# Kernel tuning notes

Measured on AMD Instinct MI355X. Metric: run time of the kernel, lower is better.

The kernel has to match this reference:

```python
import jax, jax.numpy as jnp
import numpy as np

K_MASK = -2.3819763e+38
ROPE_BASE = 10000
QUERY_SCALE = 0.08838834764831845  # head_dim ** -0.5, head_dim=128
SOFT_CAP = 50.0
SLIDING_WINDOW = 1024
NUM_HEADS = 32
NUM_KV_HEADS = 8


def apply_rope(inputs, positions, base_frequency=ROPE_BASE):
    # inputs: [B, L, N, H], positions: [B, L]
    head_dim = inputs.shape[-1]
    fraction = 2 * jnp.arange(0, head_dim // 2) / head_dim
    timescale = base_frequency ** fraction
    sinusoid = positions[..., None] / timescale[None, None, :]
    sinusoid = sinusoid[..., None, :]  # [B, L, 1, H/2]
    sin = jnp.sin(sinusoid)
    cos = jnp.cos(sinusoid)
    first, second = jnp.split(inputs, 2, axis=-1)
    out = jnp.concatenate([first * cos - second * sin,
                           second * cos + first * sin], axis=-1)
    return out.astype(inputs.dtype)


def setup_inputs() -> dict:
    key = jax.random.key(0)
    ks = jax.random.split(key, 4)
    B, S, D, N, K, H = 1, 2048, 4096, NUM_HEADS, NUM_KV_HEADS, 128
    x = jax.random.normal(ks[0], (B, S, D), dtype=jnp.float32)
    segment_pos = jnp.broadcast_to(jnp.arange(S, dtype=jnp.int32)[None, :], (B, S))
    # causal mask [B, T, S]
    attn_mask = jnp.broadcast_to(jnp.tril(jnp.ones((S, S), dtype=bool))[None], (B, S, S))
    sd = 1.0 / np.sqrt(D)
    q_w = jax.random.normal(ks[1], (N, D, H), dtype=jnp.float32) * sd
    kv_w = jax.random.normal(ks[2], (2, K, D, H), dtype=jnp.float32) * sd
    out_w = jax.random.normal(ks[3], (N, H, D), dtype=jnp.float32) * (1.0 / np.sqrt(N * H))
    return {"x": x, "segment_pos": segment_pos, "attn_mask": attn_mask,
            "q_w": q_w, "kv_w": kv_w, "out_w": out_w}


def reference(x, segment_pos, attn_mask, q_w, kv_w, out_w):
    B, T, D = x.shape
    N, _, H = q_w.shape
    K = kv_w.shape[1]
    G = N // K

    q = jnp.einsum('BTD,NDH->BTNH', x, q_w)
    k = jnp.einsum('BSD,KDH->BSKH', x, kv_w[0])
    v = jnp.einsum('BSD,KDH->BSKH', x, kv_w[1])

    q = apply_rope(q, segment_pos)
    q = q * QUERY_SCALE
    k = apply_rope(k, segment_pos)

    # GQA logits: [B, T, K, G, S] -> [B, T, N, S]
    qg = q.reshape(B, T, K, G, H)
    logits = jnp.einsum('BTKGH,BSKH->BTKGS', qg, k).reshape(B, T, N, T)

    # soft cap
    logits = jnp.tanh(logits / SOFT_CAP) * SOFT_CAP

    # sliding-window mask (no cache: end_index=0, cache positions = arange)
    cache_positions = jnp.arange(T)[None, None, :]          # [1, 1, S]
    sp = segment_pos[:, :, None]                             # [B, T, 1]
    sliding = (cache_positions > sp - SLIDING_WINDOW) & (cache_positions < sp + SLIDING_WINDOW)
    mask = attn_mask & sliding                               # [B, T, S]

    padded = jnp.where(mask[:, :, None, :], logits, K_MASK)
    probs = jax.nn.softmax(padded, axis=-1).astype(k.dtype)

    pg = probs.reshape(B, T, K, G, T)
    encoded = jnp.einsum('BTKGS,BSKH->BTKGH', pg, v).reshape(B, T, N, H)
    out = jnp.einsum('BTNH,NHD->BTD', encoded, out_w)
    return out
```

## Files before the change

### kernel.cpp

```cpp
#include <hip/hip_runtime.h>
#include <stdint.h>

#define SEQ     2048
#define DMODEL  4096
#define NHEADS  32
#define NKV     8
#define HD      128
#define NQKV    6144
#define K_MASK_F (-2.3819763e+38f)
#define QSCALE   0.08838834764831845f

typedef __attribute__((ext_vector_type(8))) short short8;
typedef __attribute__((ext_vector_type(4))) short short4v;
typedef __attribute__((ext_vector_type(4))) float f32x4;

__device__ __forceinline__ short f2bf(float f) {
  unsigned u = __float_as_uint(f);
  unsigned r = (u + 0x7fffu + ((u >> 16) & 1u)) >> 16;
  return (short)r;
}
__device__ __forceinline__ float bf2f(short s) {
  return __uint_as_float(((unsigned)(unsigned short)s) << 16);
}
__device__ __forceinline__ void split_bf(float v, short& h, short& l) {
  h = f2bf(v);
  l = f2bf(v - bf2f(h));
}
__device__ __forceinline__ f32x4 mfma16(short8 a, short8 b, f32x4 c) {
  return __builtin_amdgcn_mfma_f32_16x16x32_bf16(a, b, c, 0, 0, 0);
}
__device__ __forceinline__ void async16(void* lds, const void* g) {
  __builtin_amdgcn_global_load_lds(
      (const __attribute__((address_space(1))) unsigned int*)g,
      (__attribute__((address_space(3))) unsigned int*)lds, 16, 0, 0);
}
__device__ __forceinline__ float softcap(float s) {
  float e = __expf(s * 0.04f);
  return 50.f - 100.f * __builtin_amdgcn_rcpf(e + 1.f);
}

__global__ void cvt_split_kernel(const float* __restrict__ src, short* __restrict__ hi,
                                 short* __restrict__ lo, int n4) {
  int i = blockIdx.x * blockDim.x + threadIdx.x;
  if (i >= n4) return;
  float4 v = ((const float4*)src)[i];
  float vv[4] = {v.x, v.y, v.z, v.w};
  short hh[4], ll[4];
#pragma unroll
  for (int j = 0; j < 4; ++j) split_bf(vv[j], hh[j], ll[j]);
  short4v h = {hh[0], hh[1], hh[2], hh[3]};
  short4v l = {ll[0], ll[1], ll[2], ll[3]};
  ((short4v*)hi)[i] = h;
  ((short4v*)lo)[i] = l;
}

__global__ void tcvt_kernel(const float* __restrict__ src, long srcSlab, int srcStride,
                            short* __restrict__ dhi, short* __restrict__ dlo,
                            long dstSlab, int dstStride) {
  __shared__ float tile[32][33];
  const float* s = src + (long)blockIdx.z * srcSlab;
  long dbase = (long)blockIdx.z * dstSlab;
  int tx = threadIdx.x & 31, ty = threadIdx.x >> 5;
  int c0 = blockIdx.x * 32, r0 = blockIdx.y * 32;
#pragma unroll
  for (int i = 0; i < 32; i += 8)
    tile[ty + i][tx] = s[(long)(r0 + ty + i) * srcStride + (c0 + tx)];
  __syncthreads();
#pragma unroll
  for (int i = 0; i < 32; i += 8) {
    float v = tile[tx][ty + i];
    long o = dbase + (long)(c0 + ty + i) * dstStride + (r0 + tx);
    short h, l;
    split_bf(v, h, l);
    dhi[o] = h;
    dlo[o] = l;
  }
}

__global__ __launch_bounds__(256)
void gemm3_kernel(const short* __restrict__ Ah, const short* __restrict__ Al,
                  const short* __restrict__ Bh, const short* __restrict__ Bl,
                  float* __restrict__ C, int K, int ldc) {
  __shared__ short lds[4 * 128 * 32];
  const int tid = threadIdx.x;
  const int wave = tid >> 6, lane = tid & 63;
  const int r16 = lane & 15, g4 = lane >> 4;
  const int bm = blockIdx.x, bn = blockIdx.y;
  const int wr = wave >> 1, wc = wave & 1;

  const f32x4 zero = {0.f, 0.f, 0.f, 0.f};
  f32x4 acc[4][4];
#pragma unroll
  for (int m = 0; m < 4; ++m)
#pragma unroll
    for (int n = 0; n < 4; ++n) acc[m][n] = zero;

  const short* gsrc[4] = {Ah, Al, Bh, Bl};
  const int rowbase[4] = {bm * 128, bm * 128, bn * 128, bn * 128};
  const int stgrow = tid >> 2;
  const int stgseg = tid & 3;
  const int nk = K >> 5;

  for (int kt = 0; kt < nk; ++kt) {
    __syncthreads();
#pragma unroll
    for (int b = 0; b < 4; ++b) {
#pragma unroll
      for (int rnd = 0; rnd < 2; ++rnd) {
        int row = rnd * 64 + stgrow;
        const short* g = gsrc[b] + (long)(rowbase[b] + row) * K + kt * 32 + stgseg * 8;
        short* l = lds + b * 4096 + rnd * 2048 + wave * 512;
        async16(l, g);
      }
    }
    __syncthreads();

    short8 afh[4], afl[4], bfh[4], bfl[4];
#pragma unroll
    for (int m = 0; m < 4; ++m) {
      int r = wr * 64 + m * 16 + r16;
      afh[m] = *(const short8*)&lds[0 * 4096 + r * 32 + g4 * 8];
      afl[m] = *(const short8*)&lds[1 * 4096 + r * 32 + g4 * 8];
    }
#pragma unroll
    for (int n = 0; n < 4; ++n) {
      int r = wc * 64 + n * 16 + r16;
      bfh[n] = *(const short8*)&lds[2 * 4096 + r * 32 + g4 * 8];
      bfl[n] = *(const short8*)&lds[3 * 4096 + r * 32 + g4 * 8];
    }
#pragma unroll
    for (int m = 0; m < 4; ++m)
#pragma unroll
      for (int n = 0; n < 4; ++n) {
        acc[m][n] = mfma16(afh[m], bfh[n], acc[m][n]);
        acc[m][n] = mfma16(afh[m], bfl[n], acc[m][n]);
        acc[m][n] = mfma16(afl[m], bfh[n], acc[m][n]);
      }
  }
#pragma unroll
  for (int m = 0; m < 4; ++m)
#pragma unroll
    for (int n = 0; n < 4; ++n) {
      int row = bm * 128 + wr * 64 + m * 16 + g4 * 4;
      int col = bn * 128 + wc * 64 + n * 16 + r16;
#pragma unroll
      for (int r = 0; r < 4; ++r) C[(long)(row + r) * ldc + col] = acc[m][n][r];
    }
}

__global__ void rope_cvt_kernel(const float* __restrict__ qkv, short* __restrict__ qh,
                                short* __restrict__ ql, short* __restrict__ kh,
                                short* __restrict__ kl) {
  int idx = blockIdx.x * 256 + threadIdx.x;
  const int QP = NHEADS * SEQ * 64;
  float first, second, scale;
  long obase;
  int t, hp;
  short *oh, *ol;
  if (idx < QP) {
    int n = idx >> 17;
    int rem = idx & 131071;
    t = rem >> 6;
    hp = rem & 63;
    const float* p = qkv + (long)t * NQKV + n * HD + hp;
    first = p[0];
    second = p[64];
    oh = qh; ol = ql;
    obase = ((long)n * SEQ + t) * HD + hp;
    scale = QSCALE;
  } else {
    int j = idx - QP;
    int kvh = j >> 17;
    int rem = j & 131071;
    t = rem >> 6;
    hp = rem & 63;
    const float* p = qkv + (long)t * NQKV + DMODEL + kvh * HD + hp;
    first = p[0];
    second = p[64];
    oh = kh; ol = kl;
    obase = ((long)kvh * SEQ + t) * HD + hp;
    scale = 1.0f;
  }
  float ts = powf(10000.0f, (float)hp * (1.0f / 64.0f));
  float ang = (float)t / ts;
  float sn, cs;
  sincosf(ang, &sn, &cs);
  float o1 = (first * cs - second * sn) * scale;
  float o2 = (second * cs + first * sn) * scale;
  short h, l;
  split_bf(o1, h, l); oh[obase] = h;      ol[obase] = l;
  split_bf(o2, h, l); oh[obase + 64] = h; ol[obase + 64] = l;
}

__global__ __launch_bounds__(256)
void attn_kernel(const short* __restrict__ qh, const short* __restrict__ ql,
                 const short* __restrict__ kh, const short* __restrict__ kl,
                 const short* __restrict__ vth, const short* __restrict__ vtl,
                 short* __restrict__ ench, short* __restrict__ encl) {
  __shared__ short kt[2][2][32 * 128];
  __shared__ short plds[4][2][512];
  const int n = blockIdx.x;
  const int qt = (int)(__brev(blockIdx.y) >> 27);
  const int tid = threadIdx.x;
  const int wave = tid >> 6, lane = tid & 63;
  const int kv = n >> 2;
  const int T0 = qt * 64;
  const int wq0 = T0 + wave * 16;
  const int r16 = lane & 15, g4 = lane >> 4;

  short8 qfh[4], qfl[4];
  {
    const short* bh = qh + ((long)(n * SEQ + wq0 + r16)) * HD + g4 * 8;
    const short* bl = ql + ((long)(n * SEQ + wq0 + r16)) * HD + g4 * 8;
#pragma unroll
    for (int ks = 0; ks < 4; ++ks) {
      qfh[ks] = *(const short8*)(bh + ks * 32);
      qfl[ks] = *(const short8*)(bl + ks * 32);
    }
  }

  const f32x4 zero = {0.f, 0.f, 0.f, 0.f};
  f32x4 o[8];
#pragma unroll
  for (int i = 0; i < 8; ++i) o[i] = zero;
  float m[4] = {-INFINITY, -INFINITY, -INFINITY, -INFINITY};
  float lsum[4] = {0.f, 0.f, 0.f, 0.f};

  short* pwh = &plds[wave][0][0];
  short* pwl = &plds[wave][1][0];

  const int strow = tid >> 4;
  const int stcol = (((tid & 15) ^ (strow & 7)) << 3);
  const short* kgh = kh + (long)kv * SEQ * HD;
  const short* kgl = kl + (long)kv * SEQ * HD;

  int slo = T0 - 1023;
  if (slo < 0) slo = 0;
  slo &= ~31;
  const int steps = (T0 + 64 - slo) >> 5;

  auto stage = [&](int sc, int kbuf) {
#pragma unroll
    for (int c = 0; c < 2; ++c) {
      int row = c * 16 + strow;
      async16(&kt[kbuf][0][c * 2048 + tid * 8], kgh + (long)(sc + row) * HD + stcol);
      async16(&kt[kbuf][1][c * 2048 + tid * 8], kgl + (long)(sc + row) * HD + stcol);
    }
  };

  int buf = 0;
  stage(slo, 0);
  __syncthreads();

  for (int i = 0; i < steps; ++i) {
    const int sc = slo + (i << 5);
    if (i + 1 < steps) stage(sc + 32, buf ^ 1);
    const bool active = (sc <= wq0 + 15) && (sc + 31 >= wq0 - 1023);
    if (active) {
      const short* kb0 = &kt[buf][0][0];
      const short* kb1 = &kt[buf][1][0];
      f32x4 s0 = zero, s1 = zero;
#pragma unroll
      for (int ks = 0; ks < 4; ++ks) {
        const int ca = (ks * 32 + g4 * 8) ^ ((r16 & 7) << 3);
        short8 k0h = *(const short8*)&kb0[r16 * 128 + ca];
        short8 k0l = *(const short8*)&kb1[r16 * 128 + ca];
        short8 k1h = *(const short8*)&kb0[(16 + r16) * 128 + ca];
        short8 k1l = *(const short8*)&kb1[(16 + r16) * 128 + ca];
        s0 = mfma16(qfh[ks], k0h, s0);
        s1 = mfma16(qfh[ks], k1h, s1);
        s0 = mfma16(qfh[ks], k0l, s0);
        s1 = mfma16(qfh[ks], k1l, s1);
        s0 = mfma16(qfl[ks], k0h, s0);
        s1 = mfma16(qfl[ks], k1h, s1);
      }
      float p0[4], p1[4], rs[4];
      bool upd = false;
#pragma unroll
      for (int r = 0; r < 4; ++r) {
        const int t = wq0 + g4 * 4 + r;
        float v0 = softcap(s0[r]);
        float v1 = softcap(s1[r]);
        const int c0 = sc + r16, c1 = c0 + 16;
        v0 = (c0 <= t && c0 > t - 1024) ? v0 : K_MASK_F;
        v1 = (c1 <= t && c1 > t - 1024) ? v1 : K_MASK_F;
        float mx = fmaxf(v0, v1);
        mx = fmaxf(mx, __shfl_xor(mx, 1));
        mx = fmaxf(mx, __shfl_xor(mx, 2));
        mx = fmaxf(mx, __shfl_xor(mx, 4));
        mx = fmaxf(mx, __shfl_xor(mx, 8));
        const float mnew = (mx > m[r] + 8.f) ? fmaxf(mx, m[r]) : m[r];
        upd |= (mnew > m[r]);
        const float e0 = __expf(v0 - mnew);
        const float e1 = __expf(v1 - mnew);
        float sum = e0 + e1;
        sum += __shfl_xor(sum, 1);
        sum += __shfl_xor(sum, 2);
        sum += __shfl_xor(sum, 4);
        sum += __shfl_xor(sum, 8);
        rs[r] = __expf(m[r] - mnew);
        lsum[r] = lsum[r] * rs[r] + sum;
        m[r] = mnew;
        p0[r] = e0;
        p1[r] = e1;
      }
      if (__any((int)upd)) {
#pragma unroll
        for (int hf = 0; hf < 8; ++hf)
#pragma unroll
          for (int r = 0; r < 4; ++r) o[hf][r] *= rs[r];
      }
#pragma unroll
      for (int r = 0; r < 4; ++r) {
        const int prow = g4 * 4 + r;
        short sh, sl;
        const int off0 = prow * 32 + (((r16 >> 3) ^ (prow & 3)) * 8) + (r16 & 7);
        split_bf(p0[r], sh, sl);
        pwh[off0] = sh;
        pwl[off0] = sl;
        const int off1 = prow * 32 + ((((16 + r16) >> 3) ^ (prow & 3)) * 8) + (r16 & 7);
        split_bf(p1[r], sh, sl);
        pwh[off1] = sh;
        pwl[off1] = sl;
      }
      short8 pah = *(const short8*)&pwh[r16 * 32 + ((g4 ^ (r16 & 3)) * 8)];
      short8 pal = *(const short8*)&pwl[r16 * 32 + ((g4 ^ (r16 & 3)) * 8)];
#pragma unroll
      for (int hf = 0; hf < 8; ++hf) {
        const short* vrh = vth + (long)(kv * HD + hf * 16 + r16) * SEQ + sc + g4 * 8;
        const short* vrl = vtl + (long)(kv * HD + hf * 16 + r16) * SEQ + sc + g4 * 8;
        short8 vbh = *(const short8*)vrh;
        short8 vbl = *(const short8*)vrl;
        o[hf] = mfma16(pah, vbh, o[hf]);
        o[hf] = mfma16(pah, vbl, o[hf]);
        o[hf] = mfma16(pal, vbh, o[hf]);
      }
    }
    __syncthreads();
    buf ^= 1;
  }

  float inv[4];
#pragma unroll
  for (int r = 0; r < 4; ++r) inv[r] = 1.0f / lsum[r];
#pragma unroll
  for (int hf = 0; hf < 8; ++hf)
#pragma unroll
    for (int r = 0; r < 4; ++r) {
      const float val = o[hf][r] * inv[r];
      const int t = wq0 + g4 * 4 + r;
      const long off = (long)t * DMODEL + n * HD + hf * 16 + r16;
      short sh, sl;
      split_bf(val, sh, sl);
      ench[off] = sh;
      encl[off] = sl;
    }
}

extern "C" void kernel_launch(void* const* d_in, const int* in_sizes, int n_in,
                              void* d_out, int out_size, void* d_ws, size_t ws_size,
                              hipStream_t stream) {
  const float* x     = (const float*)d_in[0];
  const float* q_w   = (const float*)d_in[3];
  const float* kv_w  = (const float*)d_in[4];
  const float* out_w = (const float*)d_in[5];
  float* out = (float*)d_out;

  char* w = (char*)d_ws;
  const size_t MB = 1ull << 20;
  short* xh   = (short*)(w + 0);
  short* xl   = (short*)(w + 16 * MB);
  short* W1Th = (short*)(w + 32 * MB);
  short* W1Tl = (short*)(w + 80 * MB);
  short* W2Th = (short*)(w + 32 * MB);
  short* W2Tl = (short*)(w + 64 * MB);
  float* qkv  = (float*)(w + 128 * MB);
  short* ench = (short*)(w + 128 * MB);
  short* encl = (short*)(w + 144 * MB);
  short* qH   = (short*)(w + 176 * MB);
  short* qL   = (short*)(w + 192 * MB);
  short* kH   = (short*)(w + 208 * MB);
  short* kL   = (short*)(w + 212 * MB);
  short* vtH  = (short*)(w + 216 * MB);
  short* vtL  = (short*)(w + 220 * MB);

  cvt_split_kernel<<<8192, 256, 0, stream>>>(x, xh, xl, 2097152);
  tcvt_kernel<<<dim3(4, 128, 32), 256, 0, stream>>>(q_w, (long)4096 * 128, 128,
                                                    W1Th, W1Tl, (long)128 * 4096, 4096);
  tcvt_kernel<<<dim3(4, 128, 8), 256, 0, stream>>>(kv_w, (long)4096 * 128, 128,
                                                   W1Th + (long)4096 * 4096,
                                                   W1Tl + (long)4096 * 4096,
                                                   (long)128 * 4096, 4096);
  tcvt_kernel<<<dim3(4, 128, 8), 256, 0, stream>>>(kv_w + (long)8 * 4096 * 128,
                                                   (long)4096 * 128, 128,
                                                   W1Th + (long)5120 * 4096,
                                                   W1Tl + (long)5120 * 4096,
                                                   (long)128 * 4096, 4096);
  gemm3_kernel<<<dim3(16, 48), 256, 0, stream>>>(xh, xl, W1Th, W1Tl, qkv, 4096, 6144);
  rope_cvt_kernel<<<20480, 256, 0, stream>>>(qkv, qH, qL, kH, kL);
  tcvt_kernel<<<dim3(4, 64, 8), 256, 0, stream>>>(qkv + 5120, 128, 6144,
                                                  vtH, vtL, (long)128 * 2048, 2048);
  attn_kernel<<<dim3(32, 32), 256, 0, stream>>>(qH, qL, kH, kL, vtH, vtL, ench, encl);
  tcvt_kernel<<<dim3(128, 128, 1), 256, 0, stream>>>(out_w, 0, 4096, W2Th, W2Tl, 0, 4096);
  gemm3_kernel<<<dim3(16, 32), 256, 0, stream>>>(ench, encl, W2Th, W2Tl, out, 4096, 4096);
}
```

Before: 1.068 ms.

## Use fixed softcap max in softmax, stage V through LDS, remap block order

Because soft-capped logits are bounded by 50, the online-softmax running max and rescaling are replaced with a fixed offset of 50, and the per-step row-sum shuffles are deferred to the end. V tiles are now prefetched asynchronously into double-buffered shared memory alongside K, instead of being read from global memory inside the loop. Block-to-head and query-tile mapping is changed to group heads sharing a KV head and to balance work order. The split score accumulators also shorten MFMA dependency chains. The fixed offset relies on the cap bound and may reduce precision for rows whose logits are all far below 50.

```diff
diff --git a/kernel.cpp b/kernel.cpp
--- a/kernel.cpp
+++ b/kernel.cpp
@@ -192,15 +192,19 @@
   split_bf(o2, h, l); oh[obase + 64] = h; ol[obase + 64] = l;
 }
 
+#define VCH 1040
 __global__ __launch_bounds__(256)
 void attn_kernel(const short* __restrict__ qh, const short* __restrict__ ql,
                  const short* __restrict__ kh, const short* __restrict__ kl,
                  const short* __restrict__ vth, const short* __restrict__ vtl,
                  short* __restrict__ ench, short* __restrict__ encl) {
   __shared__ short kt[2][2][32 * 128];
+  __shared__ short vlds[2][2][4 * VCH];
   __shared__ short plds[4][2][512];
-  const int n = blockIdx.x;
-  const int qt = (int)(__brev(blockIdx.y) >> 27);
+  const int bx = blockIdx.x;
+  const int n = ((bx & 7) << 2) + (bx >> 3);
+  const int by = blockIdx.y;
+  const int qt = (by < 16) ? (16 + by) : (31 - by);
   const int tid = threadIdx.x;
   const int wave = tid >> 6, lane = tid & 63;
   const int kv = n >> 2;
@@ -223,7 +227,6 @@
   f32x4 o[8];
 #pragma unroll
   for (int i = 0; i < 8; ++i) o[i] = zero;
-  float m[4] = {-INFINITY, -INFINITY, -INFINITY, -INFINITY};
   float lsum[4] = {0.f, 0.f, 0.f, 0.f};
 
   short* pwh = &plds[wave][0][0];
@@ -233,6 +236,8 @@
   const int stcol = (((tid & 15) ^ (strow & 7)) << 3);
   const short* kgh = kh + (long)kv * SEQ * HD;
   const short* kgl = kl + (long)kv * SEQ * HD;
+  const short* vgh = vth + (long)kv * HD * SEQ;
+  const short* vgl = vtl + (long)kv * HD * SEQ;
 
   int slo = T0 - 1023;
   if (slo < 0) slo = 0;
@@ -245,6 +250,14 @@
       int row = c * 16 + strow;
       async16(&kt[kbuf][0][c * 2048 + tid * 8], kgh + (long)(sc + row) * HD + stcol);
       async16(&kt[kbuf][1][c * 2048 + tid * 8], kgl + (long)(sc + row) * HD + stcol);
+    }
+#pragma unroll
+    for (int r = 0; r < 2; ++r) {
+      int h = r * 64 + lane;
+      async16(&vlds[kbuf][0][wave * VCH + r * 512 + lane * 8],
+              vgh + (long)h * SEQ + sc + wave * 8);
+      async16(&vlds[kbuf][1][wave * VCH + r * 512 + lane * 8],
+              vgl + (long)h * SEQ + sc + wave * 8);
     }
   };
 
@@ -259,7 +272,7 @@
     if (active) {
       const short* kb0 = &kt[buf][0][0];
       const short* kb1 = &kt[buf][1][0];
-      f32x4 s0 = zero, s1 = zero;
+      f32x4 sA0 = zero, sB0 = zero, sA1 = zero, sB1 = zero;
 #pragma unroll
       for (int ks = 0; ks < 4; ++ks) {
         const int ca = (ks * 32 + g4 * 8) ^ ((r16 & 7) << 3);
@@ -267,48 +280,23 @@
         short8 k0l = *(const short8*)&kb1[r16 * 128 + ca];
         short8 k1h = *(const short8*)&kb0[(16 + r16) * 128 + ca];
         short8 k1l = *(const short8*)&kb1[(16 + r16) * 128 + ca];
-        s0 = mfma16(qfh[ks], k0h, s0);
-        s1 = mfma16(qfh[ks], k1h, s1);
-        s0 = mfma16(qfh[ks], k0l, s0);
-        s1 = mfma16(qfh[ks], k1l, s1);
-        s0 = mfma16(qfl[ks], k0h, s0);
-        s1 = mfma16(qfl[ks], k1h, s1);
-      }
-      float p0[4], p1[4], rs[4];
-      bool upd = false;
+        sA0 = mfma16(qfh[ks], k0h, sA0);
+        sA1 = mfma16(qfh[ks], k1h, sA1);
+        sB0 = mfma16(qfh[ks], k0l, sB0);
+        sB1 = mfma16(qfh[ks], k1l, sB1);
+        sB0 = mfma16(qfl[ks], k0h, sB0);
+        sB1 = mfma16(qfl[ks], k1h, sB1);
+      }
+      float p0[4], p1[4];
 #pragma unroll
       for (int r = 0; r < 4; ++r) {
         const int t = wq0 + g4 * 4 + r;
-        float v0 = softcap(s0[r]);
-        float v1 = softcap(s1[r]);
+        const float v0 = softcap(sA0[r] + sB0[r]);
+        const float v1 = softcap(sA1[r] + sB1[r]);
         const int c0 = sc + r16, c1 = c0 + 16;
-        v0 = (c0 <= t && c0 > t - 1024) ? v0 : K_MASK_F;
-        v1 = (c1 <= t && c1 > t - 1024) ? v1 : K_MASK_F;
-        float mx = fmaxf(v0, v1);
-        mx = fmaxf(mx, __shfl_xor(mx, 1));
-        mx = fmaxf(mx, __shfl_xor(mx, 2));
-        mx = fmaxf(mx, __shfl_xor(mx, 4));
-        mx = fmaxf(mx, __shfl_xor(mx, 8));
-        const float mnew = (mx > m[r] + 8.f) ? fmaxf(mx, m[r]) : m[r];
-        upd |= (mnew > m[r]);
-        const float e0 = __expf(v0 - mnew);
-        const float e1 = __expf(v1 - mnew);
-        float sum = e0 + e1;
-        sum += __shfl_xor(sum, 1);
-        sum += __shfl_xor(sum, 2);
-        sum += __shfl_xor(sum, 4);
-        sum += __shfl_xor(sum, 8);
-        rs[r] = __expf(m[r] - mnew);
-        lsum[r] = lsum[r] * rs[r] + sum;
-        m[r] = mnew;
-        p0[r] = e0;
-        p1[r] = e1;
-      }
-      if (__any((int)upd)) {
-#pragma unroll
-        for (int hf = 0; hf < 8; ++hf)
-#pragma unroll
-          for (int r = 0; r < 4; ++r) o[hf][r] *= rs[r];
+        p0[r] = (c0 <= t && c0 > t - 1024) ? __expf(v0 - 50.f) : 0.f;
+        p1[r] = (c1 <= t && c1 > t - 1024) ? __expf(v1 - 50.f) : 0.f;
+        lsum[r] += p0[r] + p1[r];
       }
 #pragma unroll
       for (int r = 0; r < 4; ++r) {
@@ -325,12 +313,13 @@
       }
       short8 pah = *(const short8*)&pwh[r16 * 32 + ((g4 ^ (r16 & 3)) * 8)];
       short8 pal = *(const short8*)&pwl[r16 * 32 + ((g4 ^ (r16 & 3)) * 8)];
+      const short* vb0 = &vlds[buf][0][0];
+      const short* vb1 = &vlds[buf][1][0];
 #pragma unroll
       for (int hf = 0; hf < 8; ++hf) {
-        const short* vrh = vth + (long)(kv * HD + hf * 16 + r16) * SEQ + sc + g4 * 8;
-        const short* vrl = vtl + (long)(kv * HD + hf * 16 + r16) * SEQ + sc + g4 * 8;
-        short8 vbh = *(const short8*)vrh;
-        short8 vbl = *(const short8*)vrl;
+        const int vo = g4 * VCH + (hf * 16 + r16) * 8;
+        short8 vbh = *(const short8*)&vb0[vo];
+        short8 vbl = *(const short8*)&vb1[vo];
         o[hf] = mfma16(pah, vbh, o[hf]);
         o[hf] = mfma16(pah, vbl, o[hf]);
         o[hf] = mfma16(pal, vbh, o[hf]);
@@ -342,7 +331,14 @@
 
   float inv[4];
 #pragma unroll
-  for (int r = 0; r < 4; ++r) inv[r] = 1.0f / lsum[r];
+  for (int r = 0; r < 4; ++r) {
+    float s = lsum[r];
+    s += __shfl_xor(s, 1);
+    s += __shfl_xor(s, 2);
+    s += __shfl_xor(s, 4);
+    s += __shfl_xor(s, 8);
+    inv[r] = 1.0f / s;
+  }
 #pragma unroll
   for (int hf = 0; hf < 8; ++hf)
 #pragma unroll
```

Result: faster. 907.6 us (-15.0%).
